# Performance work log

Measured on AMD Instinct MI355X. Metric: run time of the kernel, lower is better.

## Reference

```python
import jax, jax.numpy as jnp
import numpy as np

EMBED = 1280
H = 20
D = 64
MAX_CACHE_LEN = 2048
NEG = -1e30


def setup_inputs() -> dict:
    key = jax.random.key(0)
    ks = jax.random.split(key, 6)
    w = lambda k: jax.random.normal(k, (EMBED, EMBED), dtype=jnp.float32) * 0.02
    return {
        "hidden_states": jax.random.normal(ks[0], (1, 2048, EMBED), dtype=jnp.float32),
        "wq": w(ks[1]), "bq": jnp.zeros((EMBED,), jnp.float32),
        "wk": w(ks[2]),
        "wv": w(ks[3]), "bv": jnp.zeros((EMBED,), jnp.float32),
        "wo": w(ks[4]), "bo": jnp.zeros((EMBED,), jnp.float32),
        "pos_int": 0,
    }


def reference(hidden_states, wq, bq, wk, wv, bv, wo, bo, pos_int):
    B, T, E = hidden_states.shape
    scale = D ** -0.5
    # projections (torch Linear: x @ W^T + b); Whisper k_proj has no bias
    q = (hidden_states @ wq.T + bq).reshape(B, T, H, D).transpose(0, 2, 1, 3)
    k = (hidden_states @ wk.T).reshape(B, T, H, D).transpose(0, 2, 1, 3)
    v = (hidden_states @ wv.T + bv).reshape(B, T, H, D).transpose(0, 2, 1, 3)
    # static KV-cache update (ETKVCache.update): write k,v at [pos:pos+T]
    k_cache = jnp.zeros((B, H, MAX_CACHE_LEN, D), hidden_states.dtype)
    v_cache = jnp.zeros((B, H, MAX_CACHE_LEN, D), hidden_states.dtype)
    k_cache = jax.lax.dynamic_update_slice(k_cache, k, (0, 0, pos_int, 0))
    v_cache = jax.lax.dynamic_update_slice(v_cache, v, (0, 0, pos_int, 0))
    end_pos = pos_int + T
    k_win = k_cache[:, :, :end_pos, :]  # [B,H,S,D]
    v_win = v_cache[:, :, :end_pos, :]
    # SDPA with is_causal=True: torch uses top-left aligned tril(T, S) mask
    scores = jnp.einsum("bhtd,bhsd->bhts", q, k_win) * scale
    mask = jnp.tril(jnp.ones((T, end_pos), dtype=bool))
    scores = jnp.where(mask, scores, NEG)
    attn = jax.nn.softmax(scores, axis=-1)
    out = jnp.einsum("bhts,bhsd->bhtd", attn, v_win)
    out = out.transpose(0, 2, 1, 3).reshape(B, T, H * D)
    return out @ wo.T + bo
```

## Files before the change

### kernel.cpp

```cpp
#include <hip/hip_runtime.h>
#include <hip/hip_bf16.h>

typedef __bf16 bf16;
typedef __bf16 bf16x8 __attribute__((ext_vector_type(8)));
typedef float  f32x4  __attribute__((ext_vector_type(4)));
typedef float  f32x16 __attribute__((ext_vector_type(16)));
typedef unsigned int u32;
typedef u32 u32x4 __attribute__((ext_vector_type(4)));

#define AS1 __attribute__((address_space(1)))
#define AS3 __attribute__((address_space(3)))

#define T_LEN 2048
#define EMB   1280
#define NH    20
#define HD    64

#define NCHUNK_PER_HEAD 40

#define QSCALE 0.18033688011112042f

__device__ __forceinline__ void gl_lds16(const void* gsrc, void* ldst) {
  __builtin_amdgcn_global_load_lds((AS1 void*)const_cast<void*>(gsrc),
                                   (AS3 void*)ldst, 16, 0, 0);
}

__global__ __launch_bounds__(256) void cvt_all(
    const float* __restrict__ hs, const float* __restrict__ wq,
    const float* __restrict__ wk, const float* __restrict__ wv,
    const float* __restrict__ wo, bf16* __restrict__ out) {
  const int HS8 = T_LEN * EMB / 8;
  const int W8  = EMB * EMB / 8;
  int i = blockIdx.x * 256 + threadIdx.x;
  const float* src;
  bf16* dst;
  int off;
  if (i < HS8)              { src = hs; dst = out;                              off = i; }
  else if (i < HS8 + W8)    { src = wq; dst = out + (size_t)T_LEN * EMB;        off = i - HS8; }
  else if (i < HS8 + 2*W8)  { src = wk; dst = out + (size_t)T_LEN*EMB +   (size_t)EMB*EMB; off = i - HS8 - W8; }
  else if (i < HS8 + 3*W8)  { src = wv; dst = out + (size_t)T_LEN*EMB + 2*(size_t)EMB*EMB; off = i - HS8 - 2*W8; }
  else if (i < HS8 + 4*W8)  { src = wo; dst = out + (size_t)T_LEN*EMB + 3*(size_t)EMB*EMB; off = i - HS8 - 3*W8; }
  else return;
  const float4* p4 = (const float4*)src;
  float4 a = p4[2 * off], b = p4[2 * off + 1];
  bf16x8 o;
  o[0] = (bf16)a.x; o[1] = (bf16)a.y; o[2] = (bf16)a.z; o[3] = (bf16)a.w;
  o[4] = (bf16)b.x; o[5] = (bf16)b.y; o[6] = (bf16)b.z; o[7] = (bf16)b.w;
  *(bf16x8*)(dst + (size_t)off * 8) = o;
}

__global__ __launch_bounds__(256, 2) void gemm_qkv(
    const bf16* __restrict__ hsb,
    const bf16* __restrict__ wqb, const bf16* __restrict__ wkb,
    const bf16* __restrict__ wvb,
    const float* __restrict__ bq, const float* __restrict__ bv,
    bf16* __restrict__ Qb, bf16* __restrict__ Kb, bf16* __restrict__ VTb)
{
  constexpr int NK = EMB / 64;
  __shared__ alignas(16) bf16 As[2][128 * 64];
  __shared__ alignas(16) bf16 Bs[2][128 * 64];

  const int g = blockIdx.x & 7, local = blockIdx.x >> 3;
  const int sub = local / 10;
  const int bn = local % 10;
  const int bm = g * 2 + (sub & 1);
  const int mode = sub >> 1;
  const bf16* B = (mode == 0) ? wqb : (mode == 1) ? wkb : wvb;
  const int rowbase = bm * 128;

  const int lane = threadIdx.x & 63;
  const int w = threadIdx.x >> 6;
  const int wr = w >> 1, wc = w & 1;
  const int g4 = lane >> 4, c = lane & 15;

  const f32x4 z4 = {0.f, 0.f, 0.f, 0.f};
  f32x4 acc[4][4];
  #pragma unroll
  for (int i = 0; i < 4; ++i)
    #pragma unroll
    for (int j = 0; j < 4; ++j) acc[i][j] = z4;

  auto STAGE = [&](int b, int kt) {
    #pragma unroll
    for (int i = 0; i < 4; ++i) {
      const int call = w * 4 + i;
      const int slot = call * 1024 + lane * 16;
      const int row = slot >> 7;
      const int scb = (slot & 127) ^ ((row & 7) << 4);
      gl_lds16((const char*)hsb + (size_t)(rowbase + row) * (EMB * 2) + kt * 128 + scb,
               (char*)As[b] + call * 1024);
    }
    #pragma unroll
    for (int i = 0; i < 4; ++i) {
      const int call = w * 4 + i;
      const int slot = call * 1024 + lane * 16;
      const int row = slot >> 7;
      const int scb = (slot & 127) ^ ((row & 7) << 4);
      gl_lds16((const char*)B + (size_t)(bn * 128 + row) * (EMB * 2) + kt * 128 + scb,
               (char*)Bs[b] + call * 1024);
    }
  };

  STAGE(0, 0);
  for (int kt = 0; kt < NK; ++kt) {
    const int cur = kt & 1;
    STAGE(cur ^ 1, kt + 1 < NK ? kt + 1 : kt);
    asm volatile("s_waitcnt vmcnt(8)" ::: "memory");
    __builtin_amdgcn_s_barrier();
    asm volatile("" ::: "memory");
    const bf16* Asc = As[cur];
    const bf16* Bsc = Bs[cur];
    #pragma unroll
    for (int kc = 0; kc < 2; ++kc) {
      bf16x8 af[4], bfr[4];
      #pragma unroll
      for (int mt = 0; mt < 4; ++mt) {
        const int row = wr * 64 + mt * 16 + c;
        const int off = row * 128 + ((kc * 64 + g4 * 16) ^ ((row & 7) << 4));
        af[mt] = *(const bf16x8*)((const char*)Asc + off);
      }
      #pragma unroll
      for (int nt = 0; nt < 4; ++nt) {
        const int row = wc * 64 + nt * 16 + c;
        const int off = row * 128 + ((kc * 64 + g4 * 16) ^ ((row & 7) << 4));
        bfr[nt] = *(const bf16x8*)((const char*)Bsc + off);
      }
      #pragma unroll
      for (int mt = 0; mt < 4; ++mt)
        #pragma unroll
        for (int nt = 0; nt < 4; ++nt)
          acc[mt][nt] = __builtin_amdgcn_mfma_f32_16x16x32_bf16(af[mt], bfr[nt],
                                                                acc[mt][nt], 0, 0, 0);
    }
    asm volatile("" ::: "memory");
    __builtin_amdgcn_s_barrier();
  }

  #pragma unroll
  for (int mt = 0; mt < 4; ++mt) {
    const int t0 = rowbase + wr * 64 + mt * 16 + g4 * 4;
    #pragma unroll
    for (int nt = 0; nt < 4; ++nt) {
      const int n = bn * 128 + wc * 64 + nt * 16 + c;
      const int h = n >> 6, d = n & 63;
      #pragma unroll
      for (int r = 0; r < 4; ++r) {
        const int t = t0 + r;
        float v = acc[mt][nt][r];
        if (mode == 0) {
          v = (v + bq[n]) * QSCALE;
          Qb[((size_t)h * T_LEN + t) * HD + d] = (bf16)v;
        } else if (mode == 1) {
          Kb[((size_t)h * T_LEN + t) * HD + d] = (bf16)v;
        } else {
          v += bv[n];
          VTb[((size_t)h * HD + d) * T_LEN + t] = (bf16)v;
        }
      }
    }
  }
}

__global__ __launch_bounds__(128, 2) void gemm_o(
    const bf16* __restrict__ aob, const bf16* __restrict__ wob,
    const float* __restrict__ bo, float* __restrict__ Out)
{
  constexpr int NK = EMB / 64;
  __shared__ alignas(16) bf16 As[2][64 * 64];
  __shared__ alignas(16) bf16 Bs[2][64 * 64];

  const int g = blockIdx.x & 7, local = blockIdx.x >> 3;
  const int bm = g * 4 + local / 20;
  const int bn = local % 20;
  const int rowbase = bm * 64;

  const int lane = threadIdx.x & 63;
  const int w = threadIdx.x >> 6;
  const int g4 = lane >> 4, c = lane & 15;

  const f32x4 z4 = {0.f, 0.f, 0.f, 0.f};
  f32x4 acc[2][4];
  #pragma unroll
  for (int i = 0; i < 2; ++i)
    #pragma unroll
    for (int j = 0; j < 4; ++j) acc[i][j] = z4;

  auto STAGE = [&](int b, int kt) {
    #pragma unroll
    for (int i = 0; i < 4; ++i) {
      const int call = w * 4 + i;
      const int slot = call * 1024 + lane * 16;
      const int row = slot >> 7;
      const int scb = (slot & 127) ^ ((row & 7) << 4);
      gl_lds16((const char*)aob + (size_t)(rowbase + row) * (EMB * 2) + kt * 128 + scb,
               (char*)As[b] + call * 1024);
    }
    #pragma unroll
    for (int i = 0; i < 4; ++i) {
      const int call = w * 4 + i;
      const int slot = call * 1024 + lane * 16;
      const int row = slot >> 7;
      const int scb = (slot & 127) ^ ((row & 7) << 4);
      gl_lds16((const char*)wob + (size_t)(bn * 64 + row) * (EMB * 2) + kt * 128 + scb,
               (char*)Bs[b] + call * 1024);
    }
  };

  STAGE(0, 0);
  for (int kt = 0; kt < NK; ++kt) {
    const int cur = kt & 1;
    STAGE(cur ^ 1, kt + 1 < NK ? kt + 1 : kt);
    asm volatile("s_waitcnt vmcnt(8)" ::: "memory");
    __builtin_amdgcn_s_barrier();
    asm volatile("" ::: "memory");
    const bf16* Asc = As[cur];
    const bf16* Bsc = Bs[cur];
    #pragma unroll
    for (int kc = 0; kc < 2; ++kc) {
      bf16x8 af[2], bfr[4];
      #pragma unroll
      for (int mt = 0; mt < 2; ++mt) {
        const int row = w * 32 + mt * 16 + c;
        const int off = row * 128 + ((kc * 64 + g4 * 16) ^ ((row & 7) << 4));
        af[mt] = *(const bf16x8*)((const char*)Asc + off);
      }
      #pragma unroll
      for (int nt = 0; nt < 4; ++nt) {
        const int row = nt * 16 + c;
        const int off = row * 128 + ((kc * 64 + g4 * 16) ^ ((row & 7) << 4));
        bfr[nt] = *(const bf16x8*)((const char*)Bsc + off);
      }
      #pragma unroll
      for (int mt = 0; mt < 2; ++mt)
        #pragma unroll
        for (int nt = 0; nt < 4; ++nt)
          acc[mt][nt] = __builtin_amdgcn_mfma_f32_16x16x32_bf16(af[mt], bfr[nt],
                                                                acc[mt][nt], 0, 0, 0);
    }
    asm volatile("" ::: "memory");
    __builtin_amdgcn_s_barrier();
  }

  #pragma unroll
  for (int mt = 0; mt < 2; ++mt) {
    const int t0 = rowbase + w * 32 + mt * 16 + g4 * 4;
    #pragma unroll
    for (int nt = 0; nt < 4; ++nt) {
      const int n = bn * 64 + nt * 16 + c;
      #pragma unroll
      for (int r = 0; r < 4; ++r)
        Out[(size_t)(t0 + r) * EMB + n] = acc[mt][nt][r] + bo[n];
    }
  }
}

__global__ __launch_bounds__(256, 4) void attn_fwd(
    const bf16* __restrict__ Qb, const bf16* __restrict__ Kb,
    const bf16* __restrict__ VTb, bf16* __restrict__ AOb,
    bf16* __restrict__ Pob, float* __restrict__ Pml)
{
  __shared__ alignas(16) bf16 kbuf[2][64 * 64];
  __shared__ alignas(16) bf16 vbuf[2][64 * 64];

  const int g8  = blockIdx.x & 7;
  const int ord = g8 * 100 + (blockIdx.x >> 3);
  const int h   = ord / NCHUNK_PER_HEAD;
  const int idx = (NCHUNK_PER_HEAD - 1) - ord % NCHUNK_PER_HEAD;
  int qb, ch, nch;
  if (idx < 4)       { qb = idx;                ch = 0;      nch = 1; }
  else if (idx < 12) { int t = idx - 4;  qb = 4 + (t >> 1);  ch = t & 1;  nch = 2; }
  else if (idx < 24) { int t = idx - 12; qb = 8 + t / 3;     ch = t % 3;  nch = 3; }
  else               { int t = idx - 24; qb = 12 + (t >> 2); ch = t & 3;  nch = 4; }
  const int nj = 2 * qb + 2;
  const int j0 = ch * 8;
  const int j1 = (j0 + 8 < nj) ? j0 + 8 : nj;

  const int lane = threadIdx.x & 63;
  const int w  = threadIdx.x >> 6;
  const int l31 = lane & 31;
  const int hi  = lane >> 5;
  const int q0 = qb * 128;
  const int q  = q0 + w * 32 + l31;

  bf16x8 qf[4];
  {
    const char* qrow = (const char*)Qb + ((size_t)h * T_LEN + q) * (HD * 2);
    #pragma unroll
    for (int ds = 0; ds < 4; ++ds)
      qf[ds] = *(const bf16x8*)(qrow + ds * 32 + hi * 16);
  }

  f32x16 oacc[2];
  #pragma unroll
  for (int r = 0; r < 16; ++r) { oacc[0][r] = 0.f; oacc[1][r] = 0.f; }
  float m_r = -1e30f, ls = 0.f;

  auto STAGE = [&](int b, int j) {
    const int s0 = j * 64;
    #pragma unroll
    for (int i = 0; i < 2; ++i) {
      const int call = w * 2 + i;
      const int slot = call * 1024 + lane * 16;
      const int row = slot >> 7;
      const int col = (slot & 127) ^ ((row & 7) << 4);
      gl_lds16((const char*)Kb + ((size_t)h * T_LEN + s0 + row) * (HD * 2) + col,
               (char*)kbuf[b] + call * 1024);
      gl_lds16((const char*)VTb + (((size_t)h * HD + row) * T_LEN + s0) * 2 + col,
               (char*)vbuf[b] + call * 1024);
    }
  };

  auto AFRAG = [&](const bf16* buf, int rblk, int colb) -> bf16x8 {
    const int row = rblk * 32 + l31;
    const int off = row * 128 + ((colb + hi * 16) ^ ((row & 7) << 4));
    return *(const bf16x8*)((const char*)buf + off);
  };

  STAGE(0, j0);
  int cur = 0;
  for (int j = j0; j < j1; ++j) {
    STAGE(cur ^ 1, j + 1 < j1 ? j + 1 : j);
    asm volatile("s_waitcnt vmcnt(4)" ::: "memory");
    __builtin_amdgcn_s_barrier();
    asm volatile("" ::: "memory");

    f32x16 sv[2];
    #pragma unroll
    for (int r = 0; r < 16; ++r) { sv[0][r] = 0.f; sv[1][r] = 0.f; }
    #pragma unroll
    for (int ds = 0; ds < 4; ++ds) {
      #pragma unroll
      for (int sb = 0; sb < 2; ++sb) {
        bf16x8 kf = AFRAG(kbuf[cur], sb, ds * 32);
        sv[sb] = __builtin_amdgcn_mfma_f32_32x32x16_bf16(kf, qf[ds], sv[sb], 0, 0, 0);
      }
    }

    if (j >= 2 * qb) {
      const int s0 = j * 64;
      #pragma unroll
      for (int sb = 0; sb < 2; ++sb)
        #pragma unroll
        for (int r = 0; r < 16; ++r) {
          const int s = s0 + sb * 32 + (r & 3) + 8 * (r >> 2) + 4 * hi;
          if (s > q) sv[sb][r] = -1e30f;
        }
    }

    float pm = sv[0][0];
    #pragma unroll
    for (int r = 1; r < 16; ++r) pm = fmaxf(pm, sv[0][r]);
    #pragma unroll
    for (int r = 0; r < 16; ++r) pm = fmaxf(pm, sv[1][r]);
    pm = fmaxf(pm, __shfl_xor(pm, 32));
    if (!__all(pm <= m_r)) {
      const float mn = fmaxf(m_r, pm);
      const float sc = __builtin_amdgcn_exp2f(m_r - mn);
      m_r = mn;
      ls *= sc;
      oacc[0] *= sc;
      oacc[1] *= sc;
    }
    float ps = 0.f;
    #pragma unroll
    for (int sb = 0; sb < 2; ++sb)
      #pragma unroll
      for (int r = 0; r < 16; ++r) {
        const float p = __builtin_amdgcn_exp2f(sv[sb][r] - m_r);
        sv[sb][r] = p;
        ps += p;
      }
    ls += ps;

    u32 wds[16], xds[16];
    #pragma unroll
    for (int i = 0; i < 8; ++i) {
      asm("v_cvt_pk_bf16_f32 %0, %1, %2" : "=v"(wds[i])     : "v"(sv[0][2*i]), "v"(sv[0][2*i+1]));
      asm("v_cvt_pk_bf16_f32 %0, %1, %2" : "=v"(wds[8 + i]) : "v"(sv[1][2*i]), "v"(sv[1][2*i+1]));
    }
    #pragma unroll
    for (int i = 0; i < 16; ++i) xds[i] = (u32)__shfl_xor((int)wds[i], 32);

    #pragma unroll
    for (int ks = 0; ks < 4; ++ks) {
      const int o = (ks >> 1) * 8 + (ks & 1) * 4;
      u32x4 fw;
      fw.x = hi ? xds[o + 2] : wds[o];
      fw.y = hi ? xds[o + 3] : wds[o + 1];
      fw.z = hi ? wds[o + 2] : xds[o];
      fw.w = hi ? wds[o + 3] : xds[o + 1];
      bf16x8 pf = __builtin_bit_cast(bf16x8, fw);
      #pragma unroll
      for (int db = 0; db < 2; ++db) {
        bf16x8 vf = AFRAG(vbuf[cur], db, ks * 32);
        oacc[db] = __builtin_amdgcn_mfma_f32_32x32x16_bf16(vf, pf, oacc[db], 0, 0, 0);
      }
    }

    asm volatile("" ::: "memory");
    __builtin_amdgcn_s_barrier();
    cur ^= 1;
  }

  const float lt = ls + __shfl_xor(ls, 32);

  if (nch == 1) {
    const float inv = 1.f / lt;
    char* orow = (char*)AOb + ((size_t)q * EMB + h * HD) * 2;
    #pragma unroll
    for (int db = 0; db < 2; ++db)
      #pragma unroll
      for (int i = 0; i < 8; ++i) {
        const float lo = oacc[db][2 * i] * inv;
        const float hv = oacc[db][2 * i + 1] * inv;
        u32 pk;
        asm("v_cvt_pk_bf16_f32 %0, %1, %2" : "=v"(pk) : "v"(lo), "v"(hv));
        const int d = db * 32 + 8 * (i >> 1) + 2 * (i & 1) + 4 * hi;
        *(u32*)(orow + d * 2) = pk;
      }
  } else {
    const int pi = h * NCHUNK_PER_HEAD + idx;
    const int rowloc = w * 32 + l31;
    bf16* pr = Pob + ((size_t)pi * 128 + rowloc) * 64;
    #pragma unroll
    for (int db = 0; db < 2; ++db)
      #pragma unroll
      for (int i = 0; i < 8; ++i) {
        u32 pk;
        asm("v_cvt_pk_bf16_f32 %0, %1, %2" : "=v"(pk) : "v"(oacc[db][2*i]), "v"(oacc[db][2*i+1]));
        const int d = db * 32 + 8 * (i >> 1) + 2 * (i & 1) + 4 * hi;
        *(u32*)((char*)pr + d * 2) = pk;
      }
    if (hi == 0) {
      float* ml = Pml + ((size_t)pi * 128 + rowloc) * 2;
      ml[0] = m_r;
      ml[1] = lt;
    }
  }
}

__global__ __launch_bounds__(256) void attn_combine(
    const bf16* __restrict__ Pob, const float* __restrict__ Pml,
    bf16* __restrict__ AOb)
{
  const int gw = (blockIdx.x * 256 + threadIdx.x) >> 6;
  const int lane = threadIdx.x & 63;
  const int h  = gw / 1536;
  const int rr = gw % 1536;
  const int qb = 4 + rr / 128;
  const int rl = rr % 128;
  const int nch   = (qb < 8) ? 2 : (qb < 12) ? 3 : 4;
  const int ibase = (qb < 8) ? 4 + 2 * (qb - 4)
                   : (qb < 12) ? 12 + 3 * (qb - 8)
                   : 24 + 4 * (qb - 12);
  const int pi0 = h * NCHUNK_PER_HEAD + ibase;

  float mv[4], lv[4];
  float m = -1e30f;
  for (int c2 = 0; c2 < nch; ++c2) {
    const float* ml = Pml + ((size_t)(pi0 + c2) * 128 + rl) * 2;
    mv[c2] = ml[0];
    lv[c2] = ml[1];
    m = fmaxf(m, mv[c2]);
  }
  float acc = 0.f, l = 0.f;
  for (int c2 = 0; c2 < nch; ++c2) {
    const float sc = __builtin_amdgcn_exp2f(mv[c2] - m);
    const float ov = (float)Pob[((size_t)(pi0 + c2) * 128 + rl) * 64 + lane];
    acc += sc * ov;
    l   += sc * lv[c2];
  }
  const int qrow = qb * 128 + rl;
  AOb[(size_t)qrow * EMB + h * HD + lane] = (bf16)(acc / l);
}

extern "C" void kernel_launch(void* const* d_in, const int* in_sizes, int n_in,
                              void* d_out, int out_size, void* d_ws, size_t ws_size,
                              hipStream_t stream) {
  const float* hs = (const float*)d_in[0];
  const float* wq = (const float*)d_in[1];
  const float* bq = (const float*)d_in[2];
  const float* wk = (const float*)d_in[3];
  const float* wv = (const float*)d_in[4];
  const float* bv = (const float*)d_in[5];
  const float* wo = (const float*)d_in[6];
  const float* bo = (const float*)d_in[7];

  bf16* p = (bf16*)d_ws;
  bf16* hsb = p;  p += (size_t)T_LEN * EMB;
  bf16* wqb = p;  p += (size_t)EMB * EMB;
  bf16* wkb = p;  p += (size_t)EMB * EMB;
  bf16* wvb = p;  p += (size_t)EMB * EMB;
  bf16* wob = p;  p += (size_t)EMB * EMB;
  bf16* Qb  = p;  p += (size_t)NH * T_LEN * HD;
  bf16* Kb  = p;  p += (size_t)NH * T_LEN * HD;
  bf16* VTb = p;  p += (size_t)NH * HD * T_LEN;
  bf16* AOb = p;  p += (size_t)T_LEN * EMB;

  bf16*  Pob = (bf16*)d_ws;
  float* Pml = (float*)((char*)d_ws + (size_t)NH * NCHUNK_PER_HEAD * 128 * 64 * 2);

  const int TOT8 = T_LEN * EMB / 8 + 4 * (EMB * EMB / 8);
  cvt_all<<<(TOT8 + 255) / 256, 256, 0, stream>>>(hs, wq, wk, wv, wo, (bf16*)d_ws);

  gemm_qkv<<<dim3(480), 256, 0, stream>>>(hsb, wqb, wkb, wvb, bq, bv, Qb, Kb, VTb);
  attn_fwd<<<dim3(NH * NCHUNK_PER_HEAD), 256, 0, stream>>>(Qb, Kb, VTb, AOb, Pob, Pml);
  attn_combine<<<dim3(NH * 1536 / 4), 256, 0, stream>>>(Pob, Pml, AOb);
  gemm_o<<<dim3(640), 128, 0, stream>>>(AOb, wob, bo, (float*)d_out);
}
```

Before: 111.3 us.

## Load QKV GEMM A operand directly to registers, bypassing LDS

In the QKV projection GEMM, the hidden-state (A) tile is no longer staged through shared memory. Each wave loads its A fragments straight from global memory into double-buffered registers, while the weight (B) tile keeps LDS double-buffering. This halves LDS traffic and shared-memory footprint, which may allow more occupancy. The cost is more vector registers and uncoalesced per-lane global loads of A, since each A row is now read separately by the two waves that share it.

```diff
diff --git a/kernel.cpp b/kernel.cpp
--- a/kernel.cpp
+++ b/kernel.cpp
@@ -57,7 +57,6 @@
     bf16* __restrict__ Qb, bf16* __restrict__ Kb, bf16* __restrict__ VTb)
 {
   constexpr int NK = EMB / 64;
-  __shared__ alignas(16) bf16 As[2][128 * 64];
   __shared__ alignas(16) bf16 Bs[2][128 * 64];
 
   const int g = blockIdx.x & 7, local = blockIdx.x >> 3;
@@ -80,16 +79,9 @@
     #pragma unroll
     for (int j = 0; j < 4; ++j) acc[i][j] = z4;
 
-  auto STAGE = [&](int b, int kt) {
-    #pragma unroll
-    for (int i = 0; i < 4; ++i) {
-      const int call = w * 4 + i;
-      const int slot = call * 1024 + lane * 16;
-      const int row = slot >> 7;
-      const int scb = (slot & 127) ^ ((row & 7) << 4);
-      gl_lds16((const char*)hsb + (size_t)(rowbase + row) * (EMB * 2) + kt * 128 + scb,
-               (char*)As[b] + call * 1024);
-    }
+  const char* Abase = (const char*)hsb + (size_t)(rowbase + wr * 64 + c) * (EMB * 2) + g4 * 16;
+
+  auto STAGE_B = [&](int b, int kt) {
     #pragma unroll
     for (int i = 0; i < 4; ++i) {
       const int call = w * 4 + i;
@@ -101,40 +93,54 @@
     }
   };
 
-  STAGE(0, 0);
-  for (int kt = 0; kt < NK; ++kt) {
-    const int cur = kt & 1;
-    STAGE(cur ^ 1, kt + 1 < NK ? kt + 1 : kt);
-    asm volatile("s_waitcnt vmcnt(8)" ::: "memory");
-    __builtin_amdgcn_s_barrier();
-    asm volatile("" ::: "memory");
-    const bf16* Asc = As[cur];
-    const bf16* Bsc = Bs[cur];
-    #pragma unroll
-    for (int kc = 0; kc < 2; ++kc) {
-      bf16x8 af[4], bfr[4];
-      #pragma unroll
-      for (int mt = 0; mt < 4; ++mt) {
-        const int row = wr * 64 + mt * 16 + c;
-        const int off = row * 128 + ((kc * 64 + g4 * 16) ^ ((row & 7) << 4));
-        af[mt] = *(const bf16x8*)((const char*)Asc + off);
-      }
-      #pragma unroll
-      for (int nt = 0; nt < 4; ++nt) {
-        const int row = wc * 64 + nt * 16 + c;
-        const int off = row * 128 + ((kc * 64 + g4 * 16) ^ ((row & 7) << 4));
-        bfr[nt] = *(const bf16x8*)((const char*)Bsc + off);
-      }
-      #pragma unroll
-      for (int mt = 0; mt < 4; ++mt)
-        #pragma unroll
-        for (int nt = 0; nt < 4; ++nt)
-          acc[mt][nt] = __builtin_amdgcn_mfma_f32_16x16x32_bf16(af[mt], bfr[nt],
-                                                                acc[mt][nt], 0, 0, 0);
-    }
-    asm volatile("" ::: "memory");
-    __builtin_amdgcn_s_barrier();
-  }
+  bf16x8 afA[8], afB[8];
+
+  STAGE_B(0, 0);
+  #pragma unroll
+  for (int mt = 0; mt < 4; ++mt)
+    #pragma unroll
+    for (int kc = 0; kc < 2; ++kc)
+      afA[mt * 2 + kc] = *(const bf16x8*)(Abase + mt * (16 * EMB * 2) + kc * 64);
+
+#define QKV_STEP(CURA, NXTA, CURB, NXTB, KT)                                   \
+  {                                                                            \
+    const int ktn_ = ((KT) + 1 < NK) ? (KT) + 1 : (KT);                        \
+    STAGE_B(NXTB, ktn_);                                                       \
+    _Pragma("unroll")                                                          \
+    for (int mt = 0; mt < 4; ++mt)                                             \
+      _Pragma("unroll")                                                        \
+      for (int kc = 0; kc < 2; ++kc)                                           \
+        af##NXTA[mt * 2 + kc] = *(const bf16x8*)(Abase + mt * (16 * EMB * 2)   \
+                                + (size_t)ktn_ * 128 + kc * 64);               \
+    asm volatile("s_waitcnt vmcnt(16)" ::: "memory");                          \
+    __builtin_amdgcn_s_barrier();                                              \
+    asm volatile("" ::: "memory");                                             \
+    const bf16* Bsc = Bs[CURB];                                                \
+    _Pragma("unroll")                                                          \
+    for (int kc = 0; kc < 2; ++kc) {                                           \
+      bf16x8 bfr[4];                                                           \
+      _Pragma("unroll")                                                        \
+      for (int nt = 0; nt < 4; ++nt) {                                         \
+        const int row = wc * 64 + nt * 16 + c;                                 \
+        const int off = row * 128 + ((kc * 64 + g4 * 16) ^ ((row & 7) << 4));  \
+        bfr[nt] = *(const bf16x8*)((const char*)Bsc + off);                    \
+      }                                                                        \
+      _Pragma("unroll")                                                        \
+      for (int mt = 0; mt < 4; ++mt)                                           \
+        _Pragma("unroll")                                                      \
+        for (int nt = 0; nt < 4; ++nt)                                         \
+          acc[mt][nt] = __builtin_amdgcn_mfma_f32_16x16x32_bf16(               \
+              af##CURA[mt * 2 + kc], bfr[nt], acc[mt][nt], 0, 0, 0);           \
+    }                                                                          \
+    asm volatile("" ::: "memory");                                             \
+    __builtin_amdgcn_s_barrier();                                              \
+  }
+
+  for (int kt = 0; kt < NK; kt += 2) {
+    QKV_STEP(A, B, 0, 1, kt);
+    QKV_STEP(B, A, 1, 0, kt + 1);
+  }
+#undef QKV_STEP
 
   #pragma unroll
   for (int mt = 0; mt < 4; ++mt) {
```

Result: slower. 133.7 us (+20.1%).
